# Kernel tuning notes

Measured on AMD Instinct MI355X. Metric: run time of the kernel, lower is better.

Reference implementation:

```python
import jax, jax.numpy as jnp
import numpy as np

DIM = 768
NUM_HEADS = 24
WS = 8
SHIFT = 4
HID = 3072
HW = 96
EPS = 1e-5


def _rel_pos_index(ws):
    coords = np.stack(np.meshgrid(np.arange(ws), np.arange(ws), indexing='ij')).reshape(2, -1)
    rel = (coords[:, :, None] - coords[:, None, :]).transpose(1, 2, 0) + (ws - 1)
    rel[:, :, 0] *= 2 * ws - 1
    return rel.sum(-1).reshape(-1)  # (N*N,)


def _shift_mask(Hp, Wp, ws, shift):
    img = np.zeros((Hp, Wp))
    cnt = 0
    for hs in (slice(0, -ws), slice(-ws, -shift), slice(-shift, None)):
        for wsl in (slice(0, -ws), slice(-ws, -shift), slice(-shift, None)):
            img[hs, wsl] = cnt
            cnt += 1
    mw = img.reshape(Hp // ws, ws, Wp // ws, ws).transpose(0, 2, 1, 3).reshape(-1, ws * ws)
    diff = mw[:, None, :] - mw[:, :, None]
    return jnp.asarray(np.where(diff != 0, -100.0, 0.0), dtype=jnp.float32)  # (nW, N, N)


_REL_IDX = jnp.asarray(_rel_pos_index(WS))
_MASK = _shift_mask(HW, HW, WS, SHIFT)


def setup_inputs() -> dict:
    key = jax.random.key(0)
    ks = jax.random.split(key, 8)
    s = 0.02
    return {
        'x_chw': jax.random.normal(ks[0], (DIM, HW, HW), jnp.float32),
        'norm1_w': jnp.ones((DIM,), jnp.float32),
        'norm1_b': jnp.zeros((DIM,), jnp.float32),
        'qkv_w': jax.random.normal(ks[1], (3 * DIM, DIM), jnp.float32) * s,
        'qkv_b': jnp.zeros((3 * DIM,), jnp.float32),
        'proj_w': jax.random.normal(ks[2], (DIM, DIM), jnp.float32) * s,
        'proj_b': jnp.zeros((DIM,), jnp.float32),
        'bias_table': jax.random.normal(ks[3], ((2 * WS - 1) ** 2, NUM_HEADS), jnp.float32),
        'norm2_w': jnp.ones((DIM,), jnp.float32),
        'norm2_b': jnp.zeros((DIM,), jnp.float32),
        'fc1_w': jax.random.normal(ks[4], (HID, DIM), jnp.float32) * s,
        'fc1_b': jnp.zeros((HID,), jnp.float32),
        'fc2_w': jax.random.normal(ks[5], (DIM, HID), jnp.float32) * s,
        'fc2_b': jnp.zeros((DIM,), jnp.float32),
    }


def _ln_chw(x, g, b):
    # LayerNorm over channel axis at each spatial location; x: (C,H,W)
    mu = x.mean(axis=0, keepdims=True)
    var = x.var(axis=0, keepdims=True)
    return (x - mu) * jax.lax.rsqrt(var + EPS) * g[:, None, None] + b[:, None, None]


def reference(x_chw, norm1_w, norm1_b, qkv_w, qkv_b, proj_w, proj_b, bias_table,
              norm2_w, norm2_b, fc1_w, fc1_b, fc2_w, fc2_b):
    C, H, W = x_chw.shape
    Hh, dh, N = NUM_HEADS, C // NUM_HEADS, WS * WS
    scale = 1.0 / np.sqrt(dh)

    x_norm = _ln_chw(x_chw, norm1_w, norm1_b)
    x_shift = jnp.roll(x_norm, shift=(-SHIFT, -SHIFT), axis=(1, 2))
    x_hwc = jnp.moveaxis(x_shift, 0, -1)  # (H,W,C); H,W divisible by WS -> no pad

    nWh, nWw = H // WS, W // WS
    xw = x_hwc.reshape(nWh, WS, nWw, WS, C).transpose(0, 2, 1, 3, 4).reshape(nWh * nWw, N, C)

    qkv = xw @ qkv_w.T + qkv_b  # (nW, N, 3C)
    q, k, v = jnp.split(qkv, 3, axis=-1)

    def to_heads(t):
        return t.reshape(-1, N, Hh, dh).transpose(0, 2, 1, 3)  # (nW, Hh, N, dh)

    q, k, v = to_heads(q), to_heads(k), to_heads(v)
    attn = jnp.einsum('whnd,whmd->whnm', q * scale, k)
    bias = bias_table[_REL_IDX].reshape(N, N, Hh).transpose(2, 0, 1)  # (Hh, N, N)
    attn = attn + bias[None] + _MASK[:, None, :, :]
    attn = jax.nn.softmax(attn, axis=-1)
    out = jnp.einsum('whnm,whmd->whnd', attn, v)
    out = out.transpose(0, 2, 1, 3).reshape(-1, N, C)
    out = out @ proj_w.T + proj_b

    x_hwc = out.reshape(nWh, nWw, WS, WS, C).transpose(0, 2, 1, 3, 4).reshape(H, W, C)
    x_merge = jnp.moveaxis(x_hwc, -1, 0)
    x_merge = jnp.roll(x_merge, shift=(SHIFT, SHIFT), axis=(1, 2))

    x = x_chw + x_merge
    x2 = _ln_chw(x, norm2_w, norm2_b)
    tok = jnp.moveaxis(x2, 0, -1).reshape(H * W, C)
    tok = jax.nn.gelu(tok @ fc1_w.T + fc1_b) @ fc2_w.T + fc2_b
    x2 = jnp.moveaxis(tok.reshape(H, W, C), -1, 0)
    return x + x2
```

## Files before the change

### kernel.cpp

```cpp
#include <hip/hip_runtime.h>
#include <hip/hip_bf16.h>


typedef __attribute__((ext_vector_type(8))) short bf16x8;
typedef __attribute__((ext_vector_type(4))) float f32x4;

__device__ __forceinline__ short f2bf(float f){
  unsigned u = __builtin_bit_cast(unsigned, f);
  unsigned r = (u + 0x7FFFu + ((u >> 16) & 1u)) >> 16;
  return (short)r;
}
__device__ __forceinline__ float bf2f(short s){
  unsigned u = ((unsigned)(unsigned short)s) << 16;
  return __builtin_bit_cast(float, u);
}
__device__ __forceinline__ float gelu_tanh(float v){
  const float c = 0.7978845608028654f;
  float u = c * (v + 0.044715f * v * v * v);
  float e = __expf(2.f * u);
  float th = 1.f - 2.f / (e + 1.f);
  return 0.5f * v * (1.f + th);
}
__device__ __forceinline__ void gl2lds16(const short* g, short* l){
  __builtin_amdgcn_global_load_lds(
      (const __attribute__((address_space(1))) int*)g,
      (__attribute__((address_space(3))) int*)l, 16, 0, 0);
}

__global__ void k_f2b(const float* __restrict__ in, short* __restrict__ out, int n){
  int i = blockIdx.x * 256 + threadIdx.x;
  if (i < n) out[i] = f2bf(in[i]);
}

__global__ void k_bias_pre(const float* __restrict__ btab, float* __restrict__ biasp){
  int idx = blockIdx.x * 256 + threadIdx.x;
  int h = idx >> 12, mn = idx & 4095, m = mn >> 6, n = mn & 63;
  int i1 = m >> 3, j1 = m & 7, i2 = n >> 3, j2 = n & 7;
  biasp[idx] = btab[((i1 - i2 + 7) * 15 + (j1 - j2 + 7)) * 24 + h];
}

__global__ void k_ln_stats(const float* __restrict__ x, float* __restrict__ sums,
                           float* __restrict__ sumsq){
  const int p = blockIdx.x * 256 + threadIdx.x;
  const int c0 = blockIdx.y * 64;
  float s = 0.f, s2 = 0.f;
  for (int c = c0; c < c0 + 64; ++c){
    float v = x[(long)c * 9216 + p];
    s += v; s2 += v * v;
  }
  atomicAdd(&sums[p], s);
  atomicAdd(&sumsq[p], s2);
}
__global__ void k_ln_fin(const float* __restrict__ sums, const float* __restrict__ sumsq,
                         float* __restrict__ mean, float* __restrict__ rstd){
  const int p = blockIdx.x * 256 + threadIdx.x;
  float m = sums[p] * (1.f / 768.f);
  float v = sumsq[p] * (1.f / 768.f) - m * m;
  mean[p] = m;
  rstd[p] = rsqrtf(v + 1e-5f);
}

__global__ void k_ln1_win(const float* __restrict__ x, const float* __restrict__ mean,
                          const float* __restrict__ rstd, const float* __restrict__ g,
                          const float* __restrict__ b, short* __restrict__ tok){
  __shared__ float tile[64][65];
  const int w = blockIdx.x, ct = blockIdx.y * 64;
  const int wh = w / 12, ww = w - wh * 12;
  const int t = threadIdx.x;
  for (int e = t; e < 4096; e += 256){
    const int cl = e >> 6, pix = e & 63;
    int pr = wh * 8 + (pix >> 3) + 4; if (pr >= 96) pr -= 96;
    int pc = ww * 8 + (pix & 7) + 4;  if (pc >= 96) pc -= 96;
    tile[pix][cl] = x[(long)(ct + cl) * 9216 + pr * 96 + pc];
  }
  __syncthreads();
  for (int e = t; e < 4096; e += 256){
    const int pix = e >> 6, cl = e & 63;
    int pr = wh * 8 + (pix >> 3) + 4; if (pr >= 96) pr -= 96;
    int pc = ww * 8 + (pix & 7) + 4;  if (pc >= 96) pc -= 96;
    const int p = pr * 96 + pc;
    float v = (tile[pix][cl] - mean[p]) * rstd[p] * g[ct + cl] + b[ct + cl];
    tok[(long)(w * 64 + pix) * 768 + ct + cl] = f2bf(v);
  }
}

__global__ void k_merge_win(const float* __restrict__ x, const short* __restrict__ ptok,
                            float* __restrict__ x1){
  __shared__ float tile[64][65];
  const int w = blockIdx.x, ct = blockIdx.y * 64;
  const int wh = w / 12, ww = w - wh * 12;
  const int t = threadIdx.x;
  for (int e = t; e < 4096; e += 256){
    const int pix = e >> 6, cl = e & 63;
    tile[pix][cl] = bf2f(ptok[(long)(w * 64 + pix) * 768 + ct + cl]);
  }
  __syncthreads();
  for (int e = t; e < 4096; e += 256){
    const int cl = e >> 6, pix = e & 63;
    int pr = wh * 8 + (pix >> 3) + 4; if (pr >= 96) pr -= 96;
    int pc = ww * 8 + (pix & 7) + 4;  if (pc >= 96) pc -= 96;
    const long gi = (long)(ct + cl) * 9216 + pr * 96 + pc;
    x1[gi] = x[gi] + tile[pix][cl];
  }
}

__global__ void k_ln2_raster(const float* __restrict__ x1, const float* __restrict__ mean,
                             const float* __restrict__ rstd, const float* __restrict__ g,
                             const float* __restrict__ b, short* __restrict__ tok){
  __shared__ float tile[96][65];
  const int hrow = blockIdx.x, ct = blockIdx.y * 64;
  const int t = threadIdx.x;
  for (int e = t; e < 6144; e += 256){
    const int cl = e / 96, p = e - cl * 96;
    tile[p][cl] = x1[(long)(ct + cl) * 9216 + hrow * 96 + p];
  }
  __syncthreads();
  for (int e = t; e < 6144; e += 256){
    const int p = e >> 6, cl = e & 63;
    const int gp = hrow * 96 + p;
    float v = (tile[p][cl] - mean[gp]) * rstd[gp] * g[ct + cl] + b[ct + cl];
    tok[(long)gp * 768 + ct + cl] = f2bf(v);
  }
}

__global__ void k_merge_raster(const float* __restrict__ x1, const short* __restrict__ mtok,
                               float* __restrict__ out){
  __shared__ float tile[96][65];
  const int hrow = blockIdx.x, ct = blockIdx.y * 64;
  const int t = threadIdx.x;
  for (int e = t; e < 6144; e += 256){
    const int p = e >> 6, cl = e & 63;
    tile[p][cl] = bf2f(mtok[(long)(hrow * 96 + p) * 768 + ct + cl]);
  }
  __syncthreads();
  for (int e = t; e < 6144; e += 256){
    const int cl = e / 96, p = e - cl * 96;
    const long gi = (long)(ct + cl) * 9216 + hrow * 96 + p;
    out[gi] = x1[gi] + tile[p][cl];
  }
}

__global__ __launch_bounds__(256) void k_gemm_bt(
    const short* __restrict__ A, const short* __restrict__ B,
    const float* __restrict__ bias, short* __restrict__ C,
    int N, int K, int NBN, int do_gelu)
{
  __shared__ short Al[2][4096];
  __shared__ short Bl[2][4096];
  const int tid = threadIdx.x;
  const int wave = tid >> 6, lane = tid & 63;
  const int l15 = lane & 15, lg = lane >> 4;

  const int nb = gridDim.x;
  const int q = nb >> 3, r = nb & 7;
  const int xcd = blockIdx.x & 7, loc = blockIdx.x >> 3;
  const int swz = (xcd < r ? xcd * (q + 1) : r * (q + 1) + (xcd - r) * q) + loc;
  const int bn = swz % NBN, bm = swz / NBN;

  const long Abase = (long)bm * 128 * K;
  const long Bbase = (long)bn * 128 * K;
  const int srow = tid >> 2;
  const int scol = (tid & 3) << 3;
  const int wr = (wave >> 1) * 64, wc = (wave & 1) * 64;

  f32x4 acc[4][4] = {};

  auto stage = [&](int buf, int k0){
    const short* gA = A + Abase + (long)srow * K + k0 + scol;
    const short* gB = B + Bbase + (long)srow * K + k0 + scol;
    short* lA = &Al[buf][wave * 512];
    short* lB = &Bl[buf][wave * 512];
    gl2lds16(gA, lA);
    gl2lds16(gA + (long)64 * K, lA + 2048);
    gl2lds16(gB, lB);
    gl2lds16(gB + (long)64 * K, lB + 2048);
  };

  const int NKT = K >> 5;
  stage(0, 0);
  asm volatile("s_waitcnt vmcnt(0)" ::: "memory");
  __builtin_amdgcn_s_barrier();

  int buf = 0;
  for (int kt = 0; kt < NKT; ++kt){
    if (kt + 1 < NKT) stage(buf ^ 1, (kt + 1) << 5);
    bf16x8 af[4], bfv[4];
    #pragma unroll
    for (int m = 0; m < 4; ++m)
      af[m] = *(const bf16x8*)&Al[buf][(wr + m * 16 + l15) * 32 + lg * 8];
    #pragma unroll
    for (int n2 = 0; n2 < 4; ++n2)
      bfv[n2] = *(const bf16x8*)&Bl[buf][(wc + n2 * 16 + l15) * 32 + lg * 8];
    asm volatile("s_waitcnt lgkmcnt(0)" ::: "memory");
    __builtin_amdgcn_sched_barrier(0);
    #pragma unroll
    for (int m = 0; m < 4; ++m)
      #pragma unroll
      for (int n2 = 0; n2 < 4; ++n2)
        acc[m][n2] = __builtin_amdgcn_mfma_f32_16x16x32_bf16(af[m], bfv[n2], acc[m][n2], 0, 0, 0);
    asm volatile("s_waitcnt vmcnt(0)" ::: "memory");
    __builtin_amdgcn_s_barrier();
    buf ^= 1;
  }

  const long row0 = (long)bm * 128 + wr + lg * 4;
  const int col0 = bn * 128 + wc + l15;
  #pragma unroll
  for (int m = 0; m < 4; ++m){
    #pragma unroll
    for (int n2 = 0; n2 < 4; ++n2){
      const int col = col0 + n2 * 16;
      const float bb = bias[col];
      #pragma unroll
      for (int r2 = 0; r2 < 4; ++r2){
        float v = acc[m][n2][r2] + bb;
        if (do_gelu) v = gelu_tanh(v);
        C[(row0 + m * 16 + r2) * (long)N + col] = f2bf(v);
      }
    }
  }
}

#define PSTR 72
__global__ __launch_bounds__(256) void k_attn_mfma(
    const short* __restrict__ qkv, const float* __restrict__ biasp,
    short* __restrict__ out)
{
  __shared__ short Pl[4][64 * PSTR];
  const int tid = threadIdx.x, wv = tid >> 6, lane = tid & 63;
  const int l15 = lane & 15, lg = lane >> 4;
  const int task = blockIdx.x * 4 + wv;
  const int w = task / 24, h = task - w * 24;
  const int wh = w / 12, ww = w - wh * 12;
  const long base = (long)w * 64 * 2304;
  const float scale = 0.17677669529663687f;

  bf16x8 qf[4], kf[4];
  #pragma unroll
  for (int mi = 0; mi < 4; ++mi)
    qf[mi] = *(const bf16x8*)(qkv + base + (long)(mi * 16 + l15) * 2304 + h * 32 + lg * 8);
  #pragma unroll
  for (int ni = 0; ni < 4; ++ni)
    kf[ni] = *(const bf16x8*)(qkv + base + (long)(ni * 16 + l15) * 2304 + 768 + h * 32 + lg * 8);

  f32x4 acc[4][4] = {};
  #pragma unroll
  for (int mi = 0; mi < 4; ++mi)
    #pragma unroll
    for (int ni = 0; ni < 4; ++ni)
      acc[mi][ni] = __builtin_amdgcn_mfma_f32_16x16x32_bf16(qf[mi], kf[ni], acc[mi][ni], 0, 0, 0);

  const float* bh = biasp + h * 4096;
  #pragma unroll
  for (int mi = 0; mi < 4; ++mi){
    #pragma unroll
    for (int r = 0; r < 4; ++r){
      const int m = mi * 16 + lg * 4 + r;
      const int i1 = m >> 3, j1 = m & 7;
      const int labm = ((wh == 11) ? ((i1 >= 4) ? 2 : 1) : 0) * 3
                     + ((ww == 11) ? ((j1 >= 4) ? 2 : 1) : 0);
      #pragma unroll
      for (int ni = 0; ni < 4; ++ni){
        const int n = ni * 16 + l15;
        const int i2 = n >> 3, j2 = n & 7;
        const int labn = ((wh == 11) ? ((i2 >= 4) ? 2 : 1) : 0) * 3
                       + ((ww == 11) ? ((j2 >= 4) ? 2 : 1) : 0);
        float s = acc[mi][ni][r] * scale + bh[m * 64 + n];
        if (labm != labn) s -= 100.f;
        acc[mi][ni][r] = s;
      }
    }
  }

  float inv[4][4];
  #pragma unroll
  for (int mi = 0; mi < 4; ++mi){
    #pragma unroll
    for (int r = 0; r < 4; ++r){
      float mx = fmaxf(fmaxf(acc[mi][0][r], acc[mi][1][r]),
                       fmaxf(acc[mi][2][r], acc[mi][3][r]));
      #pragma unroll
      for (int off = 1; off < 16; off <<= 1) mx = fmaxf(mx, __shfl_xor(mx, off));
      float sum = 0.f;
      #pragma unroll
      for (int ni = 0; ni < 4; ++ni){
        float e = __expf(acc[mi][ni][r] - mx);
        acc[mi][ni][r] = e;
        sum += e;
      }
      #pragma unroll
      for (int off = 1; off < 16; off <<= 1) sum += __shfl_xor(sum, off);
      inv[mi][r] = 1.f / sum;
    }
  }

  short* pw = &Pl[wv][0];
  #pragma unroll
  for (int mi = 0; mi < 4; ++mi)
    #pragma unroll
    for (int ni = 0; ni < 4; ++ni)
      #pragma unroll
      for (int r = 0; r < 4; ++r)
        pw[(mi * 16 + lg * 4 + r) * PSTR + ni * 16 + l15] = f2bf(acc[mi][ni][r]);
  __syncthreads();

  f32x4 acc2[4][2] = {};
  #pragma unroll
  for (int kk = 0; kk < 2; ++kk){
    bf16x8 pa[4], vb[2];
    #pragma unroll
    for (int mi = 0; mi < 4; ++mi)
      pa[mi] = *(const bf16x8*)&pw[(mi * 16 + l15) * PSTR + kk * 32 + lg * 8];
    #pragma unroll
    for (int dj = 0; dj < 2; ++dj){
      bf16x8 t;
      #pragma unroll
      for (int e = 0; e < 8; ++e)
        t[e] = qkv[base + (long)(kk * 32 + lg * 8 + e) * 2304 + 1536 + h * 32 + dj * 16 + l15];
      vb[dj] = t;
    }
    #pragma unroll
    for (int mi = 0; mi < 4; ++mi)
      #pragma unroll
      for (int dj = 0; dj < 2; ++dj)
        acc2[mi][dj] = __builtin_amdgcn_mfma_f32_16x16x32_bf16(pa[mi], vb[dj], acc2[mi][dj], 0, 0, 0);
  }

  #pragma unroll
  for (int mi = 0; mi < 4; ++mi){
    #pragma unroll
    for (int r = 0; r < 4; ++r){
      const int m = mi * 16 + lg * 4 + r;
      const long ob = (long)(w * 64 + m) * 768 + h * 32;
      #pragma unroll
      for (int dj = 0; dj < 2; ++dj)
        out[ob + dj * 16 + l15] = f2bf(acc2[mi][dj][r] * inv[mi][r]);
    }
  }
}

extern "C" void kernel_launch(void* const* d_in, const int* in_sizes, int n_in,
                              void* d_out, int out_size, void* d_ws, size_t ws_size,
                              hipStream_t stream)
{
  const float* x      = (const float*)d_in[0];
  const float* n1w    = (const float*)d_in[1];
  const float* n1b    = (const float*)d_in[2];
  const float* qkv_w  = (const float*)d_in[3];
  const float* qkv_b  = (const float*)d_in[4];
  const float* proj_w = (const float*)d_in[5];
  const float* proj_b = (const float*)d_in[6];
  const float* btab   = (const float*)d_in[7];
  const float* n2w    = (const float*)d_in[8];
  const float* n2b    = (const float*)d_in[9];
  const float* fc1_w  = (const float*)d_in[10];
  const float* fc1_b  = (const float*)d_in[11];
  const float* fc2_w  = (const float*)d_in[12];
  const float* fc2_b  = (const float*)d_in[13];
  float* out = (float*)d_out;
  char* ws = (char*)d_ws;

  short* WQ   = (short*)(ws + 0);
  short* WP   = (short*)(ws + 3538944);
  short* W1   = (short*)(ws + 4718592);
  short* W2   = (short*)(ws + 9437184);
  float* SUMS = (float*)(ws + 14155776);
  float* SUMSQ= (float*)(ws + 14192640);
  float* MEAN = (float*)(ws + 14229504);
  float* RSTD = (float*)(ws + 14266368);
  float* BIASP= (float*)(ws + 14303232);
  short* TOK  = (short*)(ws + 14696448);
  short* BIG  = (short*)(ws + 28852224);
  short* ATT  = (short*)(ws + 85475328);
  short* PRJ  = (short*)(ws + 99631104);
  float* X1   = (float*)(ws + 113786880);

  k_f2b<<<(2304 * 768 + 255) / 256, 256, 0, stream>>>(qkv_w, WQ, 2304 * 768);
  k_f2b<<<(768 * 768 + 255) / 256, 256, 0, stream>>>(proj_w, WP, 768 * 768);
  k_f2b<<<(3072 * 768 + 255) / 256, 256, 0, stream>>>(fc1_w, W1, 3072 * 768);
  k_f2b<<<(768 * 3072 + 255) / 256, 256, 0, stream>>>(fc2_w, W2, 768 * 3072);
  k_bias_pre<<<(24 * 4096) / 256, 256, 0, stream>>>(btab, BIASP);

  hipMemsetAsync(SUMS, 0, 2 * 9216 * 4, stream);
  k_ln_stats<<<dim3(36, 12), 256, 0, stream>>>(x, SUMS, SUMSQ);
  k_ln_fin<<<36, 256, 0, stream>>>(SUMS, SUMSQ, MEAN, RSTD);
  k_ln1_win<<<dim3(144, 12), 256, 0, stream>>>(x, MEAN, RSTD, n1w, n1b, TOK);

  k_gemm_bt<<<18 * 72, 256, 0, stream>>>(TOK, WQ, qkv_b, BIG, 2304, 768, 18, 0);
  k_attn_mfma<<<864, 256, 0, stream>>>(BIG, BIASP, ATT);
  k_gemm_bt<<<6 * 72, 256, 0, stream>>>(ATT, WP, proj_b, PRJ, 768, 768, 6, 0);
  k_merge_win<<<dim3(144, 12), 256, 0, stream>>>(x, PRJ, X1);

  hipMemsetAsync(SUMS, 0, 2 * 9216 * 4, stream);
  k_ln_stats<<<dim3(36, 12), 256, 0, stream>>>(X1, SUMS, SUMSQ);
  k_ln_fin<<<36, 256, 0, stream>>>(SUMS, SUMSQ, MEAN, RSTD);
  k_ln2_raster<<<dim3(96, 12), 256, 0, stream>>>(X1, MEAN, RSTD, n2w, n2b, TOK);

  k_gemm_bt<<<24 * 72, 256, 0, stream>>>(TOK, W1, fc1_b, BIG, 3072, 768, 24, 1);
  k_gemm_bt<<<6 * 72, 256, 0, stream>>>(BIG, W2, fc2_b, ATT, 768, 3072, 6, 0);
  k_merge_raster<<<dim3(96, 12), 256, 0, stream>>>(X1, ATT, out);
}
```

Measured before the change: 502.3 us.

## Add 256x256 8-wave pipelined GEMM for QKV/FC1 and XOR-swizzle LDS

Introduces a new GEMM kernel with 256x256 tiles, 8 waves, K-step 64, a multi-phase schedule that interleaves async global-to-LDS staging with MFMA blocks, XOR-swizzled LDS addressing and setprio around the MFMA sections. The QKV and FC1 projections now use it instead of the 128x128 kernel. The existing 128x128 kernel also gets a swizzled LDS layout to reduce bank conflicts. The larger tiles raise data reuse and cut global traffic, at the cost of more LDS (128KB per block), more registers and fewer blocks, which may leave CUs underused on the smaller grids.

```diff
diff --git a/kernel.cpp b/kernel.cpp
--- a/kernel.cpp
+++ b/kernel.cpp
@@ -160,7 +160,8 @@
   const long Abase = (long)bm * 128 * K;
   const long Bbase = (long)bn * 128 * K;
   const int srow = tid >> 2;
-  const int scol = (tid & 3) << 3;
+  const int scol = ((tid & 3) ^ ((tid >> 3) & 3)) << 3;
+  const int x3 = (l15 >> 1) & 3;
   const int wr = (wave >> 1) * 64, wc = (wave & 1) * 64;
 
   f32x4 acc[4][4] = {};
@@ -187,10 +188,10 @@
     bf16x8 af[4], bfv[4];
     #pragma unroll
     for (int m = 0; m < 4; ++m)
-      af[m] = *(const bf16x8*)&Al[buf][(wr + m * 16 + l15) * 32 + lg * 8];
+      af[m] = *(const bf16x8*)&Al[buf][(wr + m * 16 + l15) * 32 + ((lg ^ x3) << 3)];
     #pragma unroll
     for (int n2 = 0; n2 < 4; ++n2)
-      bfv[n2] = *(const bf16x8*)&Bl[buf][(wc + n2 * 16 + l15) * 32 + lg * 8];
+      bfv[n2] = *(const bf16x8*)&Bl[buf][(wc + n2 * 16 + l15) * 32 + ((lg ^ x3) << 3)];
     asm volatile("s_waitcnt lgkmcnt(0)" ::: "memory");
     __builtin_amdgcn_sched_barrier(0);
     #pragma unroll
@@ -216,6 +217,117 @@
         float v = acc[m][n2][r2] + bb;
         if (do_gelu) v = gelu_tanh(v);
         C[(row0 + m * 16 + r2) * (long)N + col] = f2bf(v);
+      }
+    }
+  }
+}
+
+__global__ __launch_bounds__(512, 2) void k_gemm8(
+    const short* __restrict__ A, const short* __restrict__ B,
+    const float* __restrict__ bias, short* __restrict__ C,
+    int N, int K, int NBN, int do_gelu)
+{
+  __shared__ short sm[65536];
+  const int tid = threadIdx.x;
+  const int w = tid >> 6, l = tid & 63;
+  const int l15 = l & 15, lg = l >> 4;
+  const int wm = w >> 2, wn = w & 3;
+  const int x7 = l15 & 7;
+
+  const int nb = gridDim.x;
+  const int q = nb >> 3, r = nb & 7;
+  const int xcd = blockIdx.x & 7, loc = blockIdx.x >> 3;
+  const int swz = (xcd < r ? xcd * (q + 1) : r * (q + 1) + (xcd - r) * q) + loc;
+  const int bn = swz % NBN, bm = swz / NBN;
+
+  const long arow0 = (long)bm * 256, brow0 = (long)bn * 256;
+  const int srow_base = w * 8 + (l >> 3);
+  const int scol = ((l & 7) ^ (l >> 3)) << 3;
+
+  f32x4 acc[8][4] = {};
+
+  auto stageH = [&](int p2, int op, int h, int k0){
+    const short* g = (op ? B + (brow0 + h * 128) * (long)K
+                         : A + (arow0 + h * 128) * (long)K) + k0 + scol;
+    short* lb = &sm[((p2 * 2 + op) * 2 + h) * 8192 + w * 512];
+    gl2lds16(g + (long)srow_base * K, lb);
+    gl2lds16(g + (long)(srow_base + 64) * K, lb + 4096);
+  };
+
+  stageH(0, 1, 0, 0);  stageH(0, 1, 1, 0);  stageH(0, 0, 0, 0);  stageH(0, 0, 1, 0);
+  stageH(1, 1, 0, 64); stageH(1, 1, 1, 64); stageH(1, 0, 0, 64);
+  asm volatile("s_waitcnt vmcnt(6)" ::: "memory");
+  __builtin_amdgcn_s_barrier();
+
+#define GPH(f0, STAGE, TAIL)                                                   \
+  {                                                                            \
+    bf16x8 afr[2][2];                                                          \
+    _Pragma("unroll")                                                          \
+    for (int fi = 0; fi < 2; ++fi){                                            \
+      const int fr = (f0) + fi;                                                \
+      const int ra = abase + ((fr >> 2) * 8192)                                \
+                   + (((fr & 3) * 32 + wm * 16 + l15) * 64);                   \
+      _Pragma("unroll")                                                        \
+      for (int ks = 0; ks < 2; ++ks)                                           \
+        afr[fi][ks] = *(const bf16x8*)&sm[ra + (((ks * 4 + lg) ^ x7) << 3)];   \
+    }                                                                          \
+    STAGE;                                                                     \
+    __builtin_amdgcn_s_barrier();                                              \
+    asm volatile("s_waitcnt lgkmcnt(0)" ::: "memory");                         \
+    __builtin_amdgcn_sched_barrier(0);                                         \
+    __builtin_amdgcn_s_setprio(1);                                             \
+    _Pragma("unroll")                                                          \
+    for (int fi = 0; fi < 2; ++fi)                                             \
+      _Pragma("unroll")                                                        \
+      for (int nf = 0; nf < 4; ++nf)                                           \
+        _Pragma("unroll")                                                      \
+        for (int ks = 0; ks < 2; ++ks)                                         \
+          acc[(f0) + fi][nf] = __builtin_amdgcn_mfma_f32_16x16x32_bf16(        \
+              afr[fi][ks], bfr[nf][ks], acc[(f0) + fi][nf], 0, 0, 0);          \
+    __builtin_amdgcn_s_setprio(0);                                             \
+    TAIL;                                                                      \
+    __builtin_amdgcn_s_barrier();                                              \
+  }
+
+  const int NT = K >> 6;
+  for (int t = 0; t < NT; ++t){
+    const int p = t & 1;
+    const int abase = p * 32768;
+    const int bbase = p * 32768 + 16384;
+    const int k2 = (t + 2) << 6;
+    const bool s2 = (t + 2 < NT);
+
+    bf16x8 bfr[4][2];
+    #pragma unroll
+    for (int nf = 0; nf < 4; ++nf){
+      const int row = wn * 64 + nf * 16 + l15;
+      const int rb = bbase + ((row >> 7) * 8192) + ((row & 127) * 64);
+      #pragma unroll
+      for (int ks = 0; ks < 2; ++ks)
+        bfr[nf][ks] = *(const bf16x8*)&sm[rb + (((ks * 4 + lg) ^ x7) << 3)];
+    }
+
+    GPH(0, if (t + 1 < NT) stageH(p ^ 1, 0, 1, (t + 1) << 6), )
+    GPH(2, if (s2) stageH(p, 1, 0, k2), )
+    GPH(4, if (s2) stageH(p, 1, 1, k2), )
+    GPH(6, if (s2) stageH(p, 0, 0, k2),
+        if (s2)              { asm volatile("s_waitcnt vmcnt(6)" ::: "memory"); } \
+        else if (t + 1 < NT) { asm volatile("s_waitcnt vmcnt(0)" ::: "memory"); })
+  }
+#undef GPH
+
+  #pragma unroll
+  for (int fr = 0; fr < 8; ++fr){
+    const long row0 = (long)bm * 256 + fr * 32 + wm * 16 + lg * 4;
+    #pragma unroll
+    for (int nf = 0; nf < 4; ++nf){
+      const int col = bn * 256 + wn * 64 + nf * 16 + l15;
+      const float bb = bias[col];
+      #pragma unroll
+      for (int r2 = 0; r2 < 4; ++r2){
+        float v = acc[fr][nf][r2] + bb;
+        if (do_gelu) v = gelu_tanh(v);
+        C[(row0 + r2) * (long)N + col] = f2bf(v);
       }
     }
   }
@@ -386,7 +498,7 @@
   k_ln_fin<<<36, 256, 0, stream>>>(SUMS, SUMSQ, MEAN, RSTD);
   k_ln1_win<<<dim3(144, 12), 256, 0, stream>>>(x, MEAN, RSTD, n1w, n1b, TOK);
 
-  k_gemm_bt<<<18 * 72, 256, 0, stream>>>(TOK, WQ, qkv_b, BIG, 2304, 768, 18, 0);
+  k_gemm8<<<9 * 36, 512, 0, stream>>>(TOK, WQ, qkv_b, BIG, 2304, 768, 9, 0);
   k_attn_mfma<<<864, 256, 0, stream>>>(BIG, BIASP, ATT);
   k_gemm_bt<<<6 * 72, 256, 0, stream>>>(ATT, WP, proj_b, PRJ, 768, 768, 6, 0);
   k_merge_win<<<dim3(144, 12), 256, 0, stream>>>(x, PRJ, X1);
@@ -396,7 +508,7 @@
   k_ln_fin<<<36, 256, 0, stream>>>(SUMS, SUMSQ, MEAN, RSTD);
   k_ln2_raster<<<dim3(96, 12), 256, 0, stream>>>(X1, MEAN, RSTD, n2w, n2b, TOK);
 
-  k_gemm_bt<<<24 * 72, 256, 0, stream>>>(TOK, W1, fc1_b, BIG, 3072, 768, 24, 1);
+  k_gemm8<<<12 * 36, 512, 0, stream>>>(TOK, W1, fc1_b, BIG, 3072, 768, 12, 1);
   k_gemm_bt<<<6 * 72, 256, 0, stream>>>(BIG, W2, fc2_b, ATT, 768, 3072, 6, 0);
   k_merge_raster<<<dim3(96, 12), 256, 0, stream>>>(X1, ATT, out);
 }
```

New measurement: 503.1 us. About the same (+0.2%).
